# Optimization experiments

Hardware: AMD Instinct MI355X
Metric: run time of the kernel (lower is better)

## Reference

```python
import jax, jax.numpy as jnp
import numpy as np

B, T, D, U = 32, 2048, 1024, 1024


def setup_inputs() -> dict:
    key = jax.random.key(0)
    ks = jax.random.split(key, 6)
    scale = 0.02
    return {
        "query": jax.random.normal(ks[0], (B, D), jnp.float32),
        "values": jax.random.normal(ks[1], (B, T, D), jnp.float32),
        "W1_k": jax.random.normal(ks[2], (D, U), jnp.float32) * scale,
        "W1_b": jnp.zeros((U,), jnp.float32),
        "W2_k": jax.random.normal(ks[3], (D, U), jnp.float32) * scale,
        "W2_b": jnp.zeros((U,), jnp.float32),
        "V_k": jax.random.normal(ks[4], (U, 1), jnp.float32) * scale,
        "V_b": jnp.zeros((1,), jnp.float32),
    }


def reference(query, values, W1_k, W1_b, W2_k, W2_b, V_k, V_b):
    # query: [B, D] -> [B, 1, U]; values: [B, T, D] -> [B, T, U]
    q_proj = (query @ W1_k + W1_b)[:, None, :]
    v_proj = jnp.einsum("btd,du->btu", values, W2_k) + W2_b
    # score: [B, T, 1]
    score = jnp.tanh(q_proj + v_proj) @ V_k + V_b
    attention_weights = jax.nn.softmax(score, axis=1)  # over time axis T
    context_vector = jnp.sum(attention_weights * values, axis=1)  # [B, D]
    return context_vector
```

## Files before the change

### kernel.cpp

```cpp
#include <hip/hip_runtime.h>

#define NB 32
#define NT 2048
#define ND 1024
#define NU 1024
#define NM (NB*NT)

using f32x4 = __attribute__((ext_vector_type(4))) float;
using s16x8 = __attribute__((ext_vector_type(8))) short;

#define BAR()    asm volatile("s_barrier" ::: "memory")
#define LGKM0()  asm volatile("s_waitcnt lgkmcnt(0)" ::: "memory")
#define LGKMC(n) asm volatile("s_waitcnt lgkmcnt(" #n ")" ::: "memory")
#define VMC(n)   asm volatile("s_waitcnt vmcnt(" #n ")" ::: "memory")
#define SB0()    __builtin_amdgcn_sched_barrier(0)

__device__ __forceinline__ unsigned short f2bf(float f) {
  unsigned u = __builtin_bit_cast(unsigned, f);
  u = u + 0x7fffu + ((u >> 16) & 1u);
  return (unsigned short)(u >> 16);
}

__device__ __forceinline__ unsigned cvtpk(float lo, float hi) {
  unsigned r;
  asm("v_cvt_pk_bf16_f32 %0, %1, %2" : "=v"(r) : "v"(lo), "v"(hi));
  return r;
}

__device__ __forceinline__ void gload_lds16(const void* g, void* l) {
  __builtin_amdgcn_global_load_lds(
      (const __attribute__((address_space(1))) unsigned int*)g,
      (__attribute__((address_space(3))) unsigned int*)l, 16, 0, 0);
}

__device__ __forceinline__ float tanh_fast(float x) {
  float e = __expf(2.0f * x);
  return 1.0f - 2.0f * __builtin_amdgcn_rcpf(e + 1.0f);
}

__device__ __forceinline__ void stageB(const unsigned short* g, unsigned short* l,
                                       int w, int lane) {
  int l2 = lane >> 2;
  int gc = (lane & 3) ^ ((lane >> 3) & 3);
#pragma unroll
  for (int i = 0; i < 2; ++i) {
    int rblk = w * 2 + i;
    gload_lds16(g + (size_t)(rblk * 16 + l2) * 1024 + gc * 8, l + rblk * 512);
  }
}

__device__ __forceinline__ void loadA(const float* g, int ktile, int row, int khalf,
                                      f32x4 (&f)[4]) {
  const float* p = g + (size_t)row * 1024 + ktile * 32 + khalf * 16;
#pragma unroll
  for (int i = 0; i < 4; ++i) f[i] = *(const f32x4*)(p + 4 * i);
}

__device__ __forceinline__ void cvtwriteA(const f32x4 (&f)[4], unsigned short* bufA,
                                          int row, int khalf) {
  unsigned pk[8];
  pk[0] = cvtpk(f[0][0], f[0][1]); pk[1] = cvtpk(f[0][2], f[0][3]);
  pk[2] = cvtpk(f[1][0], f[1][1]); pk[3] = cvtpk(f[1][2], f[1][3]);
  pk[4] = cvtpk(f[2][0], f[2][1]); pk[5] = cvtpk(f[2][2], f[2][3]);
  pk[6] = cvtpk(f[3][0], f[3][1]); pk[7] = cvtpk(f[3][2], f[3][3]);
  int s = (row >> 1) & 3;
  int c0 = (khalf * 2) ^ s, c1 = (khalf * 2 + 1) ^ s;
  *(uint4*)(bufA + (row << 5) + c0 * 8) = make_uint4(pk[0], pk[1], pk[2], pk[3]);
  *(uint4*)(bufA + (row << 5) + c1 * 8) = make_uint4(pk[4], pk[5], pk[6], pk[7]);
}

__device__ __forceinline__ s16x8 frag_read(const unsigned short* buf, int row, int lg) {
  int cr = lg ^ ((row >> 1) & 3);
  return *(const s16x8*)(buf + row * 32 + cr * 8);
}

template<bool PRE, bool CVT, bool AISS, bool BST, int VM>
__device__ __forceinline__ void tile_one(
    int kt, const float* gA, const unsigned short* gB,
    unsigned short* sA, unsigned short* sB, f32x4 (&acc)[8][4],
    s16x8 (&fa03)[4], s16x8 (&fa47)[4], s16x8 (&fb)[4], f32x4 (&aset)[4],
    int w, int lane, int wr, int wc, int l15, int lg, int arow, int akh) {
  LGKM0(); SB0();
  __builtin_amdgcn_s_setprio(1);
#pragma unroll
  for (int m = 0; m < 4; ++m)
#pragma unroll
    for (int n = 0; n < 4; ++n)
      acc[m][n] = __builtin_amdgcn_mfma_f32_16x16x32_bf16(fa03[m], fb[n], acc[m][n], 0, 0, 0);
  __builtin_amdgcn_s_setprio(0);
  SB0();
  if constexpr (VM == 6) { VMC(6); }
  else if constexpr (VM == 2) { VMC(2); }
  else if constexpr (VM == 0) { VMC(0); }
  if (CVT) {
    cvtwriteA(aset, sA + ((kt + 2) & 3) * 8192, arow, akh);
    SB0();
  }
  {
    const unsigned short* pA = sA + (kt & 3) * 8192;
#pragma unroll
    for (int i = 0; i < 4; ++i) fa47[i] = frag_read(pA, wr * 128 + (4 + i) * 16 + l15, lg);
  }
  if (CVT) { LGKMC(4); }
  BAR();
  LGKM0(); SB0();
  __builtin_amdgcn_s_setprio(1);
#pragma unroll
  for (int m = 0; m < 4; ++m)
#pragma unroll
    for (int n = 0; n < 4; ++n)
      acc[4 + m][n] = __builtin_amdgcn_mfma_f32_16x16x32_bf16(fa47[m], fb[n], acc[4 + m][n], 0, 0, 0);
  __builtin_amdgcn_s_setprio(0);
  SB0();
  if (PRE) {
    const unsigned short* qA = sA + ((kt + 1) & 3) * 8192;
    const unsigned short* qB = sB + ((kt + 1) & 3) * 8192;
#pragma unroll
    for (int i = 0; i < 4; ++i) fa03[i] = frag_read(qA, wr * 128 + i * 16 + l15, lg);
#pragma unroll
    for (int n = 0; n < 4; ++n) fb[n] = frag_read(qB, wc * 64 + n * 16 + l15, lg);
  }
  if (AISS) loadA(gA, kt + 4, arow, akh, aset);
  if (BST)  stageB(gB + (size_t)(kt + 3) * 32, sB + ((kt + 3) & 3) * 8192, w, lane);
  BAR();
}

__global__ __launch_bounds__(512, 2) void k_score_gemm(
    const float* __restrict__ values, const unsigned short* __restrict__ W2t,
    const float* __restrict__ add2, const float* __restrict__ Vk,
    float* __restrict__ score_part) {
  __shared__ unsigned short sA[32768];
  __shared__ unsigned short sB[32768];
  const int tid = threadIdx.x;
  const int w = tid >> 6, lane = tid & 63;
  const int wr = w >> 2, wc = w & 3;
  const int l15 = lane & 15, lg = lane >> 4;
  const int arow = tid >> 1, akh = tid & 1;

  const int L = blockIdx.x;
  const int g = (L & 7) * 128 + (L >> 3);
  const int mtile = g >> 2, ntile = g & 3;

  const float* gA = values + ((size_t)mtile << 18);
  const unsigned short* gB = W2t + ((size_t)ntile << 18);

  f32x4 acc[8][4] = {};
  s16x8 fa03[4], fa47[4], fb[4];
  f32x4 aset0[4], aset1[4];

  {
    f32x4 t[4];
    loadA(gA, 0, arow, akh, t);
    cvtwriteA(t, sA, arow, akh);
    loadA(gA, 1, arow, akh, t);
    cvtwriteA(t, sA + 8192, arow, akh);
    stageB(gB, sB, w, lane);
    stageB(gB + 32, sB + 8192, w, lane);
    stageB(gB + 64, sB + 16384, w, lane);
    loadA(gA, 2, arow, akh, aset0);
    loadA(gA, 3, arow, akh, aset1);
    VMC(8);
    LGKM0();
    BAR();
  }
#pragma unroll
  for (int i = 0; i < 4; ++i) fa03[i] = frag_read(sA, wr * 128 + i * 16 + l15, lg);
#pragma unroll
  for (int n = 0; n < 4; ++n) fb[n] = frag_read(sB, wc * 64 + n * 16 + l15, lg);

#pragma unroll 1
  for (int kt = 0; kt < 28; kt += 2) {
    tile_one<1, 1, 1, 1, 6>(kt,     gA, gB, sA, sB, acc, fa03, fa47, fb, aset0,
                            w, lane, wr, wc, l15, lg, arow, akh);
    tile_one<1, 1, 1, 1, 6>(kt + 1, gA, gB, sA, sB, acc, fa03, fa47, fb, aset1,
                            w, lane, wr, wc, l15, lg, arow, akh);
  }
  tile_one<1, 1, 0, 1, 6>(28, gA, gB, sA, sB, acc, fa03, fa47, fb, aset0,
                          w, lane, wr, wc, l15, lg, arow, akh);
  tile_one<1, 1, 0, 0, 2>(29, gA, gB, sA, sB, acc, fa03, fa47, fb, aset1,
                          w, lane, wr, wc, l15, lg, arow, akh);
  tile_one<1, 0, 0, 0, 0>(30, gA, gB, sA, sB, acc, fa03, fa47, fb, aset0,
                          w, lane, wr, wc, l15, lg, arow, akh);
  tile_one<0, 0, 0, 0, -1>(31, gA, gB, sA, sB, acc, fa03, fa47, fb, aset1,
                           w, lane, wr, wc, l15, lg, arow, akh);

  const int b = (mtile * 256) >> 11;
  float vks[4], adds[4];
#pragma unroll
  for (int n = 0; n < 4; ++n) {
    int u = ntile * 256 + wc * 64 + n * 16 + l15;
    vks[n] = Vk[u];
    adds[n] = add2[(b << 10) + u];
  }
  __syncthreads();
  float* part = (float*)sA;
#pragma unroll
  for (int m = 0; m < 8; ++m) {
#pragma unroll
    for (int j = 0; j < 4; ++j) {
      float s = 0.f;
#pragma unroll
      for (int n = 0; n < 4; ++n) {
        float x = acc[m][n][j] + adds[n];
        s = fmaf(tanh_fast(x), vks[n], s);
      }
#pragma unroll
      for (int off = 1; off < 16; off <<= 1) s += __shfl_xor(s, off);
      if (l15 == 0) part[wc * 256 + wr * 128 + m * 16 + lg * 4 + j] = s;
    }
  }
  __syncthreads();
  if (tid < 256) {
    float v = part[tid] + part[256 + tid] + part[512 + tid] + part[768 + tid];
    score_part[((size_t)ntile << 16) + mtile * 256 + tid] = v;
  }
}

__global__ void k_qproj(const float* __restrict__ q, const float* __restrict__ W1,
                        const float* __restrict__ W1b, const float* __restrict__ W2b,
                        float* __restrict__ add2) {
  int u = blockIdx.x * 256 + threadIdx.x;
  int b = blockIdx.y;
  const float* qr = q + (b << 10);
  float s = 0.f;
#pragma unroll 8
  for (int d = 0; d < ND; ++d) s = fmaf(qr[d], W1[d * NU + u], s);
  add2[(b << 10) + u] = s + W1b[u] + W2b[u];
}

__global__ void k_w2t(const float* __restrict__ W2, unsigned short* __restrict__ W2t) {
  __shared__ unsigned short tile[64][65];
  int bu = blockIdx.x * 64, bd = blockIdx.y * 64;
  int x = threadIdx.x & 63, y4 = threadIdx.x >> 6;
#pragma unroll
  for (int r = 0; r < 16; ++r) {
    int dl = y4 * 16 + r;
    tile[x][dl] = f2bf(W2[(size_t)(bd + dl) * NU + bu + x]);
  }
  __syncthreads();
#pragma unroll
  for (int r = 0; r < 16; ++r) {
    int ul = y4 * 16 + r;
    W2t[(size_t)(bu + ul) * ND + bd + x] = tile[ul][x];
  }
}

__global__ void k_softmax(const float* __restrict__ sp, float* __restrict__ w) {
  __shared__ float redm[4], reds[4];
  int b = blockIdx.x, tid = threadIdx.x;
  float s[8];
  float mx = -1e30f;
#pragma unroll
  for (int i = 0; i < 8; ++i) {
    int t = i * 256 + tid;
    float v = 0.f;
#pragma unroll
    for (int p = 0; p < 4; ++p) v += sp[((size_t)p << 16) + (b << 11) + t];
    s[i] = v;
    mx = fmaxf(mx, v);
  }
#pragma unroll
  for (int o = 1; o < 64; o <<= 1) mx = fmaxf(mx, __shfl_xor(mx, o));
  if ((tid & 63) == 0) redm[tid >> 6] = mx;
  __syncthreads();
  mx = fmaxf(fmaxf(redm[0], redm[1]), fmaxf(redm[2], redm[3]));
  float sum = 0.f;
#pragma unroll
  for (int i = 0; i < 8; ++i) { s[i] = __expf(s[i] - mx); sum += s[i]; }
#pragma unroll
  for (int o = 1; o < 64; o <<= 1) sum += __shfl_xor(sum, o);
  if ((tid & 63) == 0) reds[tid >> 6] = sum;
  __syncthreads();
  float inv = 1.0f / (reds[0] + reds[1] + reds[2] + reds[3]);
#pragma unroll
  for (int i = 0; i < 8; ++i) w[(b << 11) + i * 256 + tid] = s[i] * inv;
}

__global__ void k_context(const float* __restrict__ values, const float* __restrict__ wv,
                          float* __restrict__ part) {
  int d4 = threadIdx.x;
  int b = blockIdx.y, tc = blockIdx.z;
  const float4* vb = (const float4*)(values + ((size_t)b << 21) + ((size_t)tc << 17)) + d4;
  const float* wb = wv + (b << 11) + (tc << 7);
  float ax = 0.f, ay = 0.f, az = 0.f, aw = 0.f;
#pragma unroll 4
  for (int t = 0; t < 128; ++t) {
    float4 v = vb[(size_t)t << 8];
    float wt = wb[t];
    ax = fmaf(wt, v.x, ax); ay = fmaf(wt, v.y, ay);
    az = fmaf(wt, v.z, az); aw = fmaf(wt, v.w, aw);
  }
  float4* po = (float4*)(part + (((size_t)tc * NB + b) << 10)) + d4;
  *po = make_float4(ax, ay, az, aw);
}

__global__ void k_ctx_reduce(const float* __restrict__ part, float* __restrict__ out) {
  int i = blockIdx.x * 256 + threadIdx.x;
  float s = 0.f;
#pragma unroll
  for (int p = 0; p < 16; ++p) s += part[(p << 15) + i];
  out[i] = s;
}

extern "C" void kernel_launch(void* const* d_in, const int* in_sizes, int n_in,
                              void* d_out, int out_size, void* d_ws, size_t ws_size,
                              hipStream_t stream) {
  const float* query  = (const float*)d_in[0];
  const float* values = (const float*)d_in[1];
  const float* W1k    = (const float*)d_in[2];
  const float* W1b    = (const float*)d_in[3];
  const float* W2k    = (const float*)d_in[4];
  const float* W2b    = (const float*)d_in[5];
  const float* Vk     = (const float*)d_in[6];
  float* out = (float*)d_out;
  char* ws = (char*)d_ws;

  size_t off = 0;
  float* add2 = (float*)(ws + off); off += (size_t)NB * NU * 4;
  float* sp   = (float*)(ws + off); off += (size_t)4 * NM * 4;
  float* wv   = (float*)(ws + off); off += (size_t)NM * 4;
  float* ctxp = (float*)(ws + off); off += (size_t)16 * NB * ND * 4;
  unsigned short* W2t = (unsigned short*)(ws + off); off += (size_t)NU * ND * 2;

  k_qproj<<<dim3(4, 32), 256, 0, stream>>>(query, W1k, W1b, W2b, add2);
  k_w2t<<<dim3(16, 16), 256, 0, stream>>>(W2k, W2t);
  k_score_gemm<<<dim3(1024), 512, 0, stream>>>(values, W2t, add2, Vk, sp);
  k_softmax<<<dim3(32), 256, 0, stream>>>(sp, wv);
  k_context<<<dim3(1, 32, 16), 256, 0, stream>>>(values, wv, ctxp);
  k_ctx_reduce<<<dim3(128), 256, 0, stream>>>(ctxp, out);
}
```

Baseline: 314.9 us.

## Pre-convert values to bf16 and restructure GEMM into 8-phase async LDS pipeline

Adds a separate pass that converts the fp32 values tensor to bf16 in workspace. The score GEMM then stages both A and B straight into LDS with global_load_lds, instead of loading A into registers and converting it in-loop. The main loop becomes a K=64 double-buffered schedule of eight phases, each interleaving a half-tile stage with a slice of MFMAs. The goal is to cut VGPR pressure and conversion work in the GEMM loop. The cost is an extra full read of fp32 values plus a write and re-read of a 128MB bf16 copy, and many more barriers.

```diff
diff --git a/kernel.cpp b/kernel.cpp
--- a/kernel.cpp
+++ b/kernel.cpp
@@ -11,9 +11,10 @@
 
 #define BAR()    asm volatile("s_barrier" ::: "memory")
 #define LGKM0()  asm volatile("s_waitcnt lgkmcnt(0)" ::: "memory")
-#define LGKMC(n) asm volatile("s_waitcnt lgkmcnt(" #n ")" ::: "memory")
 #define VMC(n)   asm volatile("s_waitcnt vmcnt(" #n ")" ::: "memory")
 #define SB0()    __builtin_amdgcn_sched_barrier(0)
+#define P1()     __builtin_amdgcn_s_setprio(1)
+#define P0()     __builtin_amdgcn_s_setprio(0)
 
 __device__ __forceinline__ unsigned short f2bf(float f) {
   unsigned u = __builtin_bit_cast(unsigned, f);
@@ -21,12 +22,6 @@
   return (unsigned short)(u >> 16);
 }
 
-__device__ __forceinline__ unsigned cvtpk(float lo, float hi) {
-  unsigned r;
-  asm("v_cvt_pk_bf16_f32 %0, %1, %2" : "=v"(r) : "v"(lo), "v"(hi));
-  return r;
-}
-
 __device__ __forceinline__ void gload_lds16(const void* g, void* l) {
   __builtin_amdgcn_global_load_lds(
       (const __attribute__((address_space(1))) unsigned int*)g,
@@ -38,151 +33,123 @@
   return 1.0f - 2.0f * __builtin_amdgcn_rcpf(e + 1.0f);
 }
 
-__device__ __forceinline__ void stageB(const unsigned short* g, unsigned short* l,
-                                       int w, int lane) {
-  int l2 = lane >> 2;
-  int gc = (lane & 3) ^ ((lane >> 3) & 3);
+__device__ __forceinline__ void stage_half(const unsigned short* g, int kt, int h,
+                                           unsigned short* lds, int w, int r3, int c8s) {
 #pragma unroll
   for (int i = 0; i < 2; ++i) {
-    int rblk = w * 2 + i;
-    gload_lds16(g + (size_t)(rblk * 16 + l2) * 1024 + gc * 8, l + rblk * 512);
-  }
-}
-
-__device__ __forceinline__ void loadA(const float* g, int ktile, int row, int khalf,
-                                      f32x4 (&f)[4]) {
-  const float* p = g + (size_t)row * 1024 + ktile * 32 + khalf * 16;
-#pragma unroll
-  for (int i = 0; i < 4; ++i) f[i] = *(const f32x4*)(p + 4 * i);
-}
-
-__device__ __forceinline__ void cvtwriteA(const f32x4 (&f)[4], unsigned short* bufA,
-                                          int row, int khalf) {
-  unsigned pk[8];
-  pk[0] = cvtpk(f[0][0], f[0][1]); pk[1] = cvtpk(f[0][2], f[0][3]);
-  pk[2] = cvtpk(f[1][0], f[1][1]); pk[3] = cvtpk(f[1][2], f[1][3]);
-  pk[4] = cvtpk(f[2][0], f[2][1]); pk[5] = cvtpk(f[2][2], f[2][3]);
-  pk[6] = cvtpk(f[3][0], f[3][1]); pk[7] = cvtpk(f[3][2], f[3][3]);
-  int s = (row >> 1) & 3;
-  int c0 = (khalf * 2) ^ s, c1 = (khalf * 2 + 1) ^ s;
-  *(uint4*)(bufA + (row << 5) + c0 * 8) = make_uint4(pk[0], pk[1], pk[2], pk[3]);
-  *(uint4*)(bufA + (row << 5) + c1 * 8) = make_uint4(pk[4], pk[5], pk[6], pk[7]);
-}
-
-__device__ __forceinline__ s16x8 frag_read(const unsigned short* buf, int row, int lg) {
-  int cr = lg ^ ((row >> 1) & 3);
-  return *(const s16x8*)(buf + row * 32 + cr * 8);
-}
-
-template<bool PRE, bool CVT, bool AISS, bool BST, int VM>
-__device__ __forceinline__ void tile_one(
-    int kt, const float* gA, const unsigned short* gB,
+    int cb = i * 8 + w;
+    gload_lds16(g + ((size_t)(h * 128 + cb * 8 + r3) << 10) + kt * 64 + c8s * 8,
+                lds + h * 8192 + cb * 512);
+  }
+}
+
+#define RD_FA(base, m0) \
+  _Pragma("unroll") for (int m_ = 0; m_ < 4; ++m_) { \
+    _Pragma("unroll") for (int ks_ = 0; ks_ < 2; ++ks_) { \
+      int row_ = wr * 128 + ((m0) + m_) * 16 + l15; \
+      int c_ = (ks_ * 4 + lg) ^ (row_ & 7); \
+      fa[m_][ks_] = *(const s16x8*)((base) + row_ * 64 + c_ * 8); } }
+
+#define RD_FB(dst, base, n0) \
+  _Pragma("unroll") for (int n_ = 0; n_ < 2; ++n_) { \
+    _Pragma("unroll") for (int ks_ = 0; ks_ < 2; ++ks_) { \
+      int row_ = wc * 64 + ((n0) + n_) * 16 + l15; \
+      int c_ = (ks_ * 4 + lg) ^ (row_ & 7); \
+      (dst)[n_][ks_] = *(const s16x8*)((base) + row_ * 64 + c_ * 8); } }
+
+#define MF(mb, fbx, nb) \
+  _Pragma("unroll") for (int m_ = 0; m_ < 4; ++m_) \
+    _Pragma("unroll") for (int n_ = 0; n_ < 2; ++n_) \
+      _Pragma("unroll") for (int ks_ = 0; ks_ < 2; ++ks_) \
+        acc[(mb) + m_][(nb) + n_] = __builtin_amdgcn_mfma_f32_16x16x32_bf16( \
+            fa[m_][ks_], (fbx)[n_][ks_], acc[(mb) + m_][(nb) + n_], 0, 0, 0);
+
+template<bool TAIL>
+__device__ __forceinline__ void iter8(
+    int i, const unsigned short* gA, const unsigned short* gB,
     unsigned short* sA, unsigned short* sB, f32x4 (&acc)[8][4],
-    s16x8 (&fa03)[4], s16x8 (&fa47)[4], s16x8 (&fb)[4], f32x4 (&aset)[4],
-    int w, int lane, int wr, int wc, int l15, int lg, int arow, int akh) {
-  LGKM0(); SB0();
-  __builtin_amdgcn_s_setprio(1);
-#pragma unroll
-  for (int m = 0; m < 4; ++m)
-#pragma unroll
-    for (int n = 0; n < 4; ++n)
-      acc[m][n] = __builtin_amdgcn_mfma_f32_16x16x32_bf16(fa03[m], fb[n], acc[m][n], 0, 0, 0);
-  __builtin_amdgcn_s_setprio(0);
-  SB0();
-  if constexpr (VM == 6) { VMC(6); }
-  else if constexpr (VM == 2) { VMC(2); }
-  else if constexpr (VM == 0) { VMC(0); }
-  if (CVT) {
-    cvtwriteA(aset, sA + ((kt + 2) & 3) * 8192, arow, akh);
-    SB0();
-  }
-  {
-    const unsigned short* pA = sA + (kt & 3) * 8192;
-#pragma unroll
-    for (int i = 0; i < 4; ++i) fa47[i] = frag_read(pA, wr * 128 + (4 + i) * 16 + l15, lg);
-  }
-  if (CVT) { LGKMC(4); }
-  BAR();
-  LGKM0(); SB0();
-  __builtin_amdgcn_s_setprio(1);
-#pragma unroll
-  for (int m = 0; m < 4; ++m)
-#pragma unroll
-    for (int n = 0; n < 4; ++n)
-      acc[4 + m][n] = __builtin_amdgcn_mfma_f32_16x16x32_bf16(fa47[m], fb[n], acc[4 + m][n], 0, 0, 0);
-  __builtin_amdgcn_s_setprio(0);
-  SB0();
-  if (PRE) {
-    const unsigned short* qA = sA + ((kt + 1) & 3) * 8192;
-    const unsigned short* qB = sB + ((kt + 1) & 3) * 8192;
-#pragma unroll
-    for (int i = 0; i < 4; ++i) fa03[i] = frag_read(qA, wr * 128 + i * 16 + l15, lg);
-#pragma unroll
-    for (int n = 0; n < 4; ++n) fb[n] = frag_read(qB, wc * 64 + n * 16 + l15, lg);
-  }
-  if (AISS) loadA(gA, kt + 4, arow, akh, aset);
-  if (BST)  stageB(gB + (size_t)(kt + 3) * 32, sB + ((kt + 3) & 3) * 8192, w, lane);
-  BAR();
-}
-
-__global__ __launch_bounds__(512, 2) void k_score_gemm(
-    const float* __restrict__ values, const unsigned short* __restrict__ W2t,
+    int w, int r3, int c8s, int wr, int wc, int l15, int lg) {
+  const unsigned short* d0A = sA;
+  const unsigned short* d0B = sB;
+  const unsigned short* d1A = sA + 16384;
+  const unsigned short* d1B = sB + 16384;
+  s16x8 fa[4][2], fbA[2][2], fbB[2][2];
+  const int kt0 = 2 * i;
+  RD_FA(d0A, 0); RD_FB(fbA, d0B, 0);
+  stage_half(gA, kt0 + 1, 1, sA + 16384, w, r3, c8s);
+  BAR(); LGKM0(); SB0();
+  P1(); MF(0, fbA, 0); P0();
+  BAR();
+  RD_FB(fbB, d0B, 2);
+  stage_half(gB, kt0 + 1, 0, sB + 16384, w, r3, c8s);
+  BAR(); LGKM0(); SB0();
+  P1(); MF(0, fbB, 2); P0();
+  BAR();
+  RD_FA(d0A, 4);
+  stage_half(gB, kt0 + 1, 1, sB + 16384, w, r3, c8s);
+  BAR(); LGKM0(); SB0();
+  P1(); MF(4, fbB, 2); P0();
+  BAR();
+  if (!TAIL) { stage_half(gA, kt0 + 2, 0, sA, w, r3, c8s); VMC(2); }
+  else { VMC(0); }
+  BAR(); SB0();
+  P1(); MF(4, fbA, 0); P0();
+  BAR();
+  RD_FA(d1A, 0); RD_FB(fbA, d1B, 0);
+  if (!TAIL) stage_half(gA, kt0 + 2, 1, sA, w, r3, c8s);
+  BAR(); LGKM0(); SB0();
+  P1(); MF(0, fbA, 0); P0();
+  BAR();
+  RD_FB(fbB, d1B, 2);
+  if (!TAIL) stage_half(gB, kt0 + 2, 0, sB, w, r3, c8s);
+  BAR(); LGKM0(); SB0();
+  P1(); MF(0, fbB, 2); P0();
+  BAR();
+  RD_FA(d1A, 4);
+  if (!TAIL) stage_half(gB, kt0 + 2, 1, sB, w, r3, c8s);
+  BAR(); LGKM0(); SB0();
+  P1(); MF(4, fbB, 2); P0();
+  BAR();
+  if (!TAIL) { stage_half(gA, kt0 + 3, 0, sA + 16384, w, r3, c8s); VMC(2); }
+  BAR(); SB0();
+  P1(); MF(4, fbA, 0); P0();
+  BAR();
+}
+
+__global__ __launch_bounds__(512, 2) void k_score_gemm8(
+    const unsigned short* __restrict__ vbf, const unsigned short* __restrict__ W2t,
     const float* __restrict__ add2, const float* __restrict__ Vk,
     float* __restrict__ score_part) {
   __shared__ unsigned short sA[32768];
   __shared__ unsigned short sB[32768];
   const int tid = threadIdx.x;
-  const int w = tid >> 6, lane = tid & 63;
+  const int w = tid >> 6;
+  const int lane = tid & 63;
   const int wr = w >> 2, wc = w & 3;
   const int l15 = lane & 15, lg = lane >> 4;
-  const int arow = tid >> 1, akh = tid & 1;
+  const int r3 = lane >> 3, c8s = (lane & 7) ^ r3;
 
   const int L = blockIdx.x;
   const int g = (L & 7) * 128 + (L >> 3);
   const int mtile = g >> 2, ntile = g & 3;
 
-  const float* gA = values + ((size_t)mtile << 18);
+  const unsigned short* gA = vbf + ((size_t)mtile << 18);
   const unsigned short* gB = W2t + ((size_t)ntile << 18);
 
   f32x4 acc[8][4] = {};
-  s16x8 fa03[4], fa47[4], fb[4];
-  f32x4 aset0[4], aset1[4];
-
-  {
-    f32x4 t[4];
-    loadA(gA, 0, arow, akh, t);
-    cvtwriteA(t, sA, arow, akh);
-    loadA(gA, 1, arow, akh, t);
-    cvtwriteA(t, sA + 8192, arow, akh);
-    stageB(gB, sB, w, lane);
-    stageB(gB + 32, sB + 8192, w, lane);
-    stageB(gB + 64, sB + 16384, w, lane);
-    loadA(gA, 2, arow, akh, aset0);
-    loadA(gA, 3, arow, akh, aset1);
-    VMC(8);
-    LGKM0();
-    BAR();
-  }
-#pragma unroll
-  for (int i = 0; i < 4; ++i) fa03[i] = frag_read(sA, wr * 128 + i * 16 + l15, lg);
-#pragma unroll
-  for (int n = 0; n < 4; ++n) fb[n] = frag_read(sB, wc * 64 + n * 16 + l15, lg);
+
+  stage_half(gA, 0, 0, sA, w, r3, c8s);
+  stage_half(gA, 0, 1, sA, w, r3, c8s);
+  stage_half(gB, 0, 0, sB, w, r3, c8s);
+  stage_half(gB, 0, 1, sB, w, r3, c8s);
+  stage_half(gA, 1, 0, sA + 16384, w, r3, c8s);
+  VMC(2);
+  BAR();
 
 #pragma unroll 1
-  for (int kt = 0; kt < 28; kt += 2) {
-    tile_one<1, 1, 1, 1, 6>(kt,     gA, gB, sA, sB, acc, fa03, fa47, fb, aset0,
-                            w, lane, wr, wc, l15, lg, arow, akh);
-    tile_one<1, 1, 1, 1, 6>(kt + 1, gA, gB, sA, sB, acc, fa03, fa47, fb, aset1,
-                            w, lane, wr, wc, l15, lg, arow, akh);
-  }
-  tile_one<1, 1, 0, 1, 6>(28, gA, gB, sA, sB, acc, fa03, fa47, fb, aset0,
-                          w, lane, wr, wc, l15, lg, arow, akh);
-  tile_one<1, 1, 0, 0, 2>(29, gA, gB, sA, sB, acc, fa03, fa47, fb, aset1,
-                          w, lane, wr, wc, l15, lg, arow, akh);
-  tile_one<1, 0, 0, 0, 0>(30, gA, gB, sA, sB, acc, fa03, fa47, fb, aset0,
-                          w, lane, wr, wc, l15, lg, arow, akh);
-  tile_one<0, 0, 0, 0, -1>(31, gA, gB, sA, sB, acc, fa03, fa47, fb, aset1,
-                           w, lane, wr, wc, l15, lg, arow, akh);
+  for (int i = 0; i < 7; ++i)
+    iter8<false>(i, gA, gB, sA, sB, acc, w, r3, c8s, wr, wc, l15, lg);
+  iter8<true>(7, gA, gB, sA, sB, acc, w, r3, c8s, wr, wc, l15, lg);
 
   const int b = (mtile * 256) >> 11;
   float vks[4], adds[4];
@@ -242,6 +209,16 @@
   for (int r = 0; r < 16; ++r) {
     int ul = y4 * 16 + r;
     W2t[(size_t)(bu + ul) * ND + bd + x] = tile[ul][x];
+  }
+}
+
+__global__ void k_cvt_values(const float4* __restrict__ v, ushort4* __restrict__ o) {
+  const int n4 = NM * ND / 4;
+  for (int i = blockIdx.x * blockDim.x + threadIdx.x; i < n4; i += gridDim.x * blockDim.x) {
+    float4 f = v[i];
+    ushort4 h;
+    h.x = f2bf(f.x); h.y = f2bf(f.y); h.z = f2bf(f.z); h.w = f2bf(f.w);
+    o[i] = h;
   }
 }
 
@@ -321,10 +298,12 @@
   float* wv   = (float*)(ws + off); off += (size_t)NM * 4;
   float* ctxp = (float*)(ws + off); off += (size_t)16 * NB * ND * 4;
   unsigned short* W2t = (unsigned short*)(ws + off); off += (size_t)NU * ND * 2;
+  unsigned short* vbf = (unsigned short*)(ws + off); off += (size_t)NM * ND * 2;
 
   k_qproj<<<dim3(4, 32), 256, 0, stream>>>(query, W1k, W1b, W2b, add2);
   k_w2t<<<dim3(16, 16), 256, 0, stream>>>(W2k, W2t);
-  k_score_gemm<<<dim3(1024), 512, 0, stream>>>(values, W2t, add2, Vk, sp);
+  k_cvt_values<<<dim3(2048), 256, 0, stream>>>((const float4*)values, (ushort4*)vbf);
+  k_score_gemm8<<<dim3(1024), 512, 0, stream>>>(vbf, W2t, add2, Vk, sp);
   k_softmax<<<dim3(32), 256, 0, stream>>>(sp, wv);
   k_context<<<dim3(1, 32, 16), 256, 0, stream>>>(values, wv, ctxp);
   k_ctx_reduce<<<dim3(128), 256, 0, stream>>>(ctxp, out);
```

New measurement: 343.6 us. +9.1%, slower.
